# Kernel tuning notes

Measured on AMD Instinct MI355X. Metric: run time of the kernel, lower is better.

## Reference

```python
import jax, jax.numpy as jnp
import numpy as np

B, S, H, STEPS = 4096, 169, 64, 24  # batch, input seq (window 168 + covariate row), hidden, rollout steps


def _lstm(xseq, Wih, Whh, bih, bhh, h0, c0):
    """PyTorch-style single-layer LSTM. xseq: [B,T,D] -> ([B,T,H], hT, cT). Gate order i,f,g,o."""
    xg = jnp.einsum('btd,gd->btg', xseq, Wih) + (bih + bhh)  # precompute input proj [B,T,4H]

    def step(carry, xg_t):
        h, c = carry
        g = xg_t + h @ Whh.T
        i, f, gg, o = jnp.split(g, 4, axis=-1)
        c = jax.nn.sigmoid(f) * c + jax.nn.sigmoid(i) * jnp.tanh(gg)
        h = jax.nn.sigmoid(o) * jnp.tanh(c)
        return (h, c), h

    (hT, cT), hs = jax.lax.scan(step, (h0, c0), jnp.swapaxes(xg, 0, 1))
    return jnp.swapaxes(hs, 0, 1), hT, cT


def reference(x, Wih1, Whh1, bih1, bhh1, Wih2, Whh2, bih2, bhh2, fc1_w, fc1_b, fc2_w, fc2_b):
    win, d = x[:, :-1, :], x[:, -1, :]  # [B,168,1], [B,1]
    z = jnp.zeros((x.shape[0], H), x.dtype)

    def outer(win, _):
        h1s, h1, c1 = _lstm(win, Wih1, Whh1, bih1, bhh1, z, z)
        h1s = jax.nn.relu(h1s)
        # lstm2 is seeded with lstm1's final (h, c) state, as in the torch code
        h2s, _, _ = _lstm(h1s, Wih2, Whh2, bih2, bhh2, h1, c1)
        feat = jnp.concatenate([jax.nn.relu(h2s[:, -1, :]), d], axis=1)  # [B,65]
        out = (feat @ fc1_w.T + fc1_b) @ fc2_w.T + fc2_b  # [B,1] (no relu between fc1/fc2)
        win = jnp.concatenate([win[:, 1:, :], out[:, :, None]], axis=1)  # slide window
        return win, out[:, 0]

    _, outs = jax.lax.scan(outer, win, None, length=STEPS)  # outs: [24,B]
    return jnp.swapaxes(outs, 0, 1)  # [B,24]


def setup_inputs() -> dict:
    key = jax.random.key(0)
    ks = jax.random.split(key, 14)
    bnd = 1.0 / np.sqrt(H)

    def u(k, shape):
        return jax.random.uniform(k, shape, jnp.float32, -bnd, bnd)

    return {
        'x': jax.random.normal(ks[0], (B, S, 1), jnp.float32),
        'Wih1': u(ks[1], (4 * H, 1)),
        'Whh1': u(ks[2], (4 * H, H)),
        'bih1': u(ks[3], (4 * H,)),
        'bhh1': u(ks[4], (4 * H,)),
        'Wih2': u(ks[5], (4 * H, H)),
        'Whh2': u(ks[6], (4 * H, H)),
        'bih2': u(ks[7], (4 * H,)),
        'bhh2': u(ks[8], (4 * H,)),
        'fc1_w': u(ks[9], (64, 65)),
        'fc1_b': u(ks[10], (64,)),
        'fc2_w': u(ks[11], (1, 64)),
        'fc2_b': u(ks[12], (1,)),
    }
```

## Files before the change

### kernel.cpp

```cpp
#include <hip/hip_runtime.h>
#include <stdint.h>

#define NB 16
#define WIN 168
#define NSTEPS 24
#define NBLK (4096/NB)

typedef __attribute__((ext_vector_type(8))) short bf16x8;
typedef __attribute__((ext_vector_type(4))) float f32x4;

#if __has_builtin(__builtin_amdgcn_rcpf)
#define RCPF(x) __builtin_amdgcn_rcpf(x)
#else
#define RCPF(x) (1.0f / (x))
#endif
#if __has_builtin(__builtin_amdgcn_exp2f)
#define EXP2F(x) __builtin_amdgcn_exp2f(x)
#else
#define EXP2F(x) __expf((x) * 0.6931471805599453f)
#endif

__device__ __forceinline__ float sigm(float x){
  return RCPF(1.0f + EXP2F(x * -1.4426950408889634f));
}
__device__ __forceinline__ float tanh_(float x){
  return __builtin_fmaf(2.0f, RCPF(1.0f + EXP2F(x * -2.8853900817779268f)), -1.0f);
}

__device__ __forceinline__ uint32_t bf_rn(float f){
  uint32_t u = __builtin_bit_cast(uint32_t, f);
  return (u + 0x7FFFu + ((u >> 16) & 1u)) >> 16;
}
__device__ __forceinline__ float bf_f(uint32_t s){
  return __builtin_bit_cast(float, s << 16);
}
__device__ __forceinline__ void split_t(float f, uint32_t& hi, uint32_t& lo){
  uint32_t u = __builtin_bit_cast(uint32_t, f);
  hi = u >> 16;
  lo = bf_rn(f - bf_f(hi));
}
__device__ __forceinline__ void split_s(float f, short& hi, short& lo){
  uint32_t h = bf_rn(f);
  hi = (short)h;
  lo = (short)bf_rn(f - bf_f(h));
}
__device__ __forceinline__ f32x4 mfma16(bf16x8 a, bf16x8 b, f32x4 c){
  return __builtin_amdgcn_mfma_f32_16x16x32_bf16(a, b, c, 0, 0, 0);
}

__device__ __forceinline__ void lstm_epi(const f32x4 acc[4], float c[4], float hn[4]){
  #pragma unroll
  for (int r = 0; r < 4; r++){
    float gi = acc[0][r], gf = acc[1][r], gg = acc[2][r], go = acc[3][r];
    float cn = __builtin_fmaf(sigm(gf), c[r], sigm(gi) * tanh_(gg));
    c[r] = cn;
    hn[r] = sigm(go) * tanh_(cn);
  }
}

#define FROW 136
#define FBLK 544
#define FB(buf,hl,kt) ((((buf)*2 + (hl))*2 + (kt)) * FBLK)
#define BUF_INTS (2*FBLK)

template<bool FUSED>
__global__ __launch_bounds__(256, 1) void lstm_rec_kernel(
  const float* __restrict__ x,    const float* __restrict__ Wih1, const float* __restrict__ Whh1,
  const float* __restrict__ bih1, const float* __restrict__ bhh1,
  const float* __restrict__ Wih2, const float* __restrict__ Whh2,
  const float* __restrict__ bih2, const float* __restrict__ bhh2,
  const float* __restrict__ fc1w, const float* __restrict__ fc1b,
  const float* __restrict__ fc2w, const float* __restrict__ fc2b,
  float* __restrict__ out, short* __restrict__ hist)
{
  __shared__ __align__(16) short aS[2*2*2*FBLK];
  __shared__ __align__(16) short bS[FUSED ? 2*2*2*FBLK : 16];
  __shared__ __align__(16) short r1f[FUSED ? 16 : 2*2*2*FBLK];
  __shared__ __align__(16) short rlf[FUSED ? 16 : 2*2*2*FBLK];
  __shared__ float win_s[WIN][NB];
  __shared__ float Hlast[NB][68];
  __shared__ float fc1w_s[64*68];
  __shared__ float dval_s[NB];

  const int tid = threadIdx.x;
  const int wv  = tid >> 6;
  const int ln  = tid & 63;
  const int q   = ln >> 4;
  const int n   = ln & 15;
  const int bg0 = blockIdx.x * NB;
  const int u0  = 16*wv + 4*q;
  const int kt_  = u0 >> 5;
  const int q2_  = (u0 >> 3) & 3;
  const int jj0_ = u0 & 7;
  const int rdo  = q*FROW + n*8;
  const int wro  = q2_*FROW + n*8 + jj0_;
  const int gwo  = kt_*512 + q2_*128 + n*8 + jj0_;
  const int ro   = q*128 + n*8;
  short* __restrict__ hblk = FUSED ? (hist + (size_t)blockIdx.x * WIN * 2048) : nullptr;

  for (int i = tid; i < WIN*NB; i += 256){ int t = i >> 4, b = i & 15; win_s[t][b] = x[(bg0 + b)*169 + t]; }
  for (int i = tid; i < 64*65; i += 256){ int j = i / 65, k = i % 65; fc1w_s[j*68 + k] = fc1w[i]; }
  if (tid < NB) dval_s[tid] = x[(bg0 + tid)*169 + 168];

  const float fc1b_r = fc1b[ln];
  const float fc2w_r = fc2w[ln];
  const float fc2b_r = fc2b[0];

  bf16x8 A1hi[4][2], A1lo[4][2], Ain1[4];
  bf16x8 A2hi[4][4], A2lo[4][4];
  f32x4 b1c[4], b2c[4];
  #pragma unroll
  for (int e = 0; e < 4; e++){
    const int ja = 64*e + 16*wv + n;
    #pragma unroll
    for (int kt = 0; kt < 2; kt++){
      const float* p = Whh1 + ja*64 + kt*32 + q*8;
      #pragma unroll
      for (int jj = 0; jj < 8; jj++){ short h,l; split_s(p[jj], h, l); A1hi[e][kt][jj] = h; A1lo[e][kt][jj] = l; }
    }
    #pragma unroll
    for (int kt = 0; kt < 4; kt++){
      const float* p = (kt < 2 ? (Wih2 + ja*64 + kt*32) : (Whh2 + ja*64 + (kt-2)*32)) + q*8;
      #pragma unroll
      for (int jj = 0; jj < 8; jj++){ short h,l; split_s(p[jj], h, l); A2hi[e][kt][jj] = h; A2lo[e][kt][jj] = l; }
    }
    bf16x8 ain = {0,0,0,0,0,0,0,0};
    if (q == 0){ short wh, wl; split_s(Wih1[ja], wh, wl); ain[0] = wh; ain[1] = wh; ain[2] = wl; }
    Ain1[e] = ain;
    const int jc = 64*e + u0;
    #pragma unroll
    for (int r = 0; r < 4; r++){
      b1c[e][r] = bih1[jc+r] + bhh1[jc+r];
      b2c[e][r] = bih2[jc+r] + bhh2[jc+r];
    }
  }

  float c1[4], c2[4], c1r[4];

  auto lstm1_step = [&](short* S, float* cst, int rb, int wb, int slot, int relu_dst, int t, bool first){
    f32x4 acc[4];
    bf16x8 bin = {0,0,0,0,0,0,0,0};
    { float xv = win_s[slot][n]; uint32_t xh, xl; split_t(xv, xh, xl);
      if (q == 0){ bin[0] = (short)xh; bin[1] = (short)xl; bin[2] = (short)xh; } }
    if (first){
      #pragma unroll
      for (int e = 0; e < 4; e++) acc[e] = mfma16(Ain1[e], bin, b1c[e]);
    } else {
      bf16x8 Bh0 = *(const bf16x8*)&S[FB(rb,0,0)+rdo];
      bf16x8 Bl0 = *(const bf16x8*)&S[FB(rb,1,0)+rdo];
      bf16x8 Bh1 = *(const bf16x8*)&S[FB(rb,0,1)+rdo];
      bf16x8 Bl1 = *(const bf16x8*)&S[FB(rb,1,1)+rdo];
      #pragma unroll
      for (int e = 0; e < 4; e++){
        f32x4 a = b1c[e];
        a = mfma16(A1hi[e][0], Bh0, a);
        a = mfma16(A1hi[e][0], Bl0, a);
        a = mfma16(A1lo[e][0], Bh0, a);
        a = mfma16(A1hi[e][1], Bh1, a);
        a = mfma16(A1hi[e][1], Bl1, a);
        a = mfma16(A1lo[e][1], Bh1, a);
        a = mfma16(Ain1[e], bin, a);
        acc[e] = a;
      }
    }
    float hn[4];
    lstm_epi(acc, cst, hn);
    uint32_t ph[4], pl[4];
    #pragma unroll
    for (int r = 0; r < 4; r++) split_t(hn[r], ph[r], pl[r]);
    *(uint2*)&S[FB(wb,0,kt_)+wro] = make_uint2(ph[0] | (ph[1]<<16), ph[2] | (ph[3]<<16));
    *(uint2*)&S[FB(wb,1,kt_)+wro] = make_uint2(pl[0] | (pl[1]<<16), pl[2] | (pl[3]<<16));
    if (relu_dst){
      uint32_t sh[4], sl[4];
      #pragma unroll
      for (int r = 0; r < 4; r++){ bool pos = hn[r] > 0.0f; sh[r] = pos ? ph[r] : 0u; sl[r] = pos ? pl[r] : 0u; }
      uint2 phi = make_uint2(sh[0] | (sh[1]<<16), sh[2] | (sh[3]<<16));
      uint2 plo = make_uint2(sl[0] | (sl[1]<<16), sl[2] | (sl[3]<<16));
      if (relu_dst == 1){
        short* Hp = hblk + (size_t)t * 2048;
        *(uint2*)&Hp[gwo]        = phi;
        *(uint2*)&Hp[1024 + gwo] = plo;
      } else {
        *(uint2*)&rlf[FB(rb,0,kt_)+wro] = phi;
        *(uint2*)&rlf[FB(rb,1,kt_)+wro] = plo;
      }
    }
  };

  auto lstm2_core = [&](bf16x8 L1h0, bf16x8 L1l0, bf16x8 L1h1, bf16x8 L1l1,
                        const short* Sr, int rbuf, short* Sw, int wbuf, bool last){
    bf16x8 L2h0 = *(const bf16x8*)&Sr[FB(rbuf,0,0)+rdo];
    bf16x8 L2l0 = *(const bf16x8*)&Sr[FB(rbuf,1,0)+rdo];
    bf16x8 L2h1 = *(const bf16x8*)&Sr[FB(rbuf,0,1)+rdo];
    bf16x8 L2l1 = *(const bf16x8*)&Sr[FB(rbuf,1,1)+rdo];
    f32x4 acc[4];
    #pragma unroll
    for (int e = 0; e < 4; e++){
      f32x4 a = b2c[e];
      a = mfma16(A2hi[e][0], L1h0, a);
      a = mfma16(A2hi[e][0], L1l0, a);
      a = mfma16(A2lo[e][0], L1h0, a);
      a = mfma16(A2hi[e][1], L1h1, a);
      a = mfma16(A2hi[e][1], L1l1, a);
      a = mfma16(A2lo[e][1], L1h1, a);
      a = mfma16(A2hi[e][2], L2h0, a);
      a = mfma16(A2hi[e][2], L2l0, a);
      a = mfma16(A2lo[e][2], L2h0, a);
      a = mfma16(A2hi[e][3], L2h1, a);
      a = mfma16(A2hi[e][3], L2l1, a);
      a = mfma16(A2lo[e][3], L2h1, a);
      acc[e] = a;
    }
    float hn[4];
    lstm_epi(acc, c2, hn);
    if (!last){
      uint32_t ph[4], pl[4];
      #pragma unroll
      for (int r = 0; r < 4; r++) split_t(hn[r], ph[r], pl[r]);
      *(uint2*)&Sw[FB(wbuf,0,kt_)+wro] = make_uint2(ph[0] | (ph[1]<<16), ph[2] | (ph[3]<<16));
      *(uint2*)&Sw[FB(wbuf,1,kt_)+wro] = make_uint2(pl[0] | (pl[1]<<16), pl[2] | (pl[3]<<16));
    } else {
      #pragma unroll
      for (int r = 0; r < 4; r++) Hlast[n][u0 + r] = fmaxf(hn[r], 0.0f);
    }
  };

  auto hload = [&](int t, bf16x8& h0, bf16x8& l0, bf16x8& h1, bf16x8& l1){
    const short* Hp = hblk + (size_t)t * 2048;
    h0 = *(const bf16x8*)&Hp[ro];
    l0 = *(const bf16x8*)&Hp[1024 + ro];
    h1 = *(const bf16x8*)&Hp[512 + ro];
    l1 = *(const bf16x8*)&Hp[1536 + ro];
  };

  auto fc_head = [&](int s){
    float o4[4];
    #pragma unroll
    for (int bi = 0; bi < 4; bi++){
      const int b = 4*wv + bi;
      float a1 = fc1b_r;
      #pragma unroll
      for (int k4 = 0; k4 < 16; k4++){
        const float* wp = &fc1w_s[ln*68 + k4*4];
        const float* hp = &Hlast[b][k4*4];
        a1 += wp[0]*hp[0] + wp[1]*hp[1] + wp[2]*hp[2] + wp[3]*hp[3];
      }
      a1 += dval_s[b] * fc1w_s[ln*68 + 64];
      float v = a1 * fc2w_r;
      #pragma unroll
      for (int off = 32; off > 0; off >>= 1) v += __shfl_xor(v, off);
      o4[bi] = v + fc2b_r;
    }
    if (ln == 0){
      #pragma unroll
      for (int bi = 0; bi < 4; bi++){
        const int b = 4*wv + bi;
        out[(bg0 + b)*24 + s] = o4[bi];
        win_s[s % WIN][b] = o4[bi];
      }
    }
  };

  if constexpr (FUSED){
    #pragma unroll
    for (int r = 0; r < 4; r++) c1[r] = 0.0f;
    __syncthreads();
    lstm1_step(aS, c1, 0, 1, 0, 1, 0, true);
    for (int t = 1; t < WIN; t++){
      __syncthreads();
      lstm1_step(aS, c1, t & 1, (t & 1) ^ 1, t, 1, t, false);
    }

    for (int sg = 1; sg < NSTEPS; sg++){
      #pragma unroll
      for (int r = 0; r < 4; r++){ c2[r] = c1[r]; c1[r] = 0.0f; }
      bf16x8 ch0, cl0, ch1, cl1, nh0, nl0, nh1, nl1;
      hload(0, ch0, cl0, ch1, cl1);
      int slot = sg;
      hload(1, nh0, nl0, nh1, nl1);
      __syncthreads();
      lstm1_step(aS, c1, 0, 1, slot, 1, 0, true);
      lstm2_core(ch0, cl0, ch1, cl1, aS, 0, bS, 1, false);
      ch0 = nh0; cl0 = nl0; ch1 = nh1; cl1 = nl1;
      slot++; if (slot == WIN) slot = 0;
      for (int t = 1; t < WIN-1; t++){
        hload(t+1, nh0, nl0, nh1, nl1);
        __syncthreads();
        lstm1_step(aS, c1, t & 1, (t & 1) ^ 1, slot, 1, t, false);
        lstm2_core(ch0, cl0, ch1, cl1, bS, t & 1, bS, (t & 1) ^ 1, false);
        ch0 = nh0; cl0 = nl0; ch1 = nh1; cl1 = nl1;
        slot++; if (slot == WIN) slot = 0;
      }
      __syncthreads();
      lstm2_core(ch0, cl0, ch1, cl1, bS, 1, bS, 0, true);
      __syncthreads();
      fc_head(sg - 1);
      __syncthreads();
      lstm1_step(aS, c1, 1, 0, slot, 1, WIN-1, false);
    }

    #pragma unroll
    for (int r = 0; r < 4; r++) c2[r] = c1[r];
    {
      bf16x8 ch0, cl0, ch1, cl1, nh0, nl0, nh1, nl1;
      hload(0, ch0, cl0, ch1, cl1);
      hload(1, nh0, nl0, nh1, nl1);
      __syncthreads();
      lstm2_core(ch0, cl0, ch1, cl1, aS, 0, bS, 1, false);
      ch0 = nh0; cl0 = nl0; ch1 = nh1; cl1 = nl1;
      for (int t = 1; t < WIN; t++){
        if (t < WIN-1) hload(t+1, nh0, nl0, nh1, nl1);
        __syncthreads();
        lstm2_core(ch0, cl0, ch1, cl1, bS, t & 1, bS, (t & 1) ^ 1, t == WIN-1);
        ch0 = nh0; cl0 = nl0; ch1 = nh1; cl1 = nl1;
      }
      __syncthreads();
      fc_head(NSTEPS - 1);
    }
  } else {
    for (int s = 0; s < NSTEPS; s++){
      { int* p = (int*)&aS[0];
        for (int i = tid; i < BUF_INTS; i += 256) p[i] = 0; }
      #pragma unroll
      for (int r = 0; r < 4; r++) c1[r] = 0.0f;
      int slot = s;
      for (int t = 0; t < WIN; t++){
        __syncthreads();
        lstm1_step(aS, c1, t & 1, (t & 1) ^ 1, slot, 0, t, false);
        slot++; if (slot == WIN) slot = 0;
      }
      #pragma unroll
      for (int r = 0; r < 4; r++){ c2[r] = c1[r]; c1r[r] = 0.0f; }
      { int* p = (int*)&r1f[0];
        for (int i = tid; i < BUF_INTS; i += 256) p[i] = 0; }
      slot = s;
      __syncthreads();
      lstm1_step(r1f, c1r, 0, 1, slot, 2, 0, false);
      slot++;
      for (int i = 1; i < WIN; i++){
        __syncthreads();
        const int rb = i & 1, wb = rb ^ 1;
        lstm1_step(r1f, c1r, rb, wb, slot, 2, i, false);
        bf16x8 L1h0 = *(const bf16x8*)&rlf[FB(wb,0,0)+rdo];
        bf16x8 L1l0 = *(const bf16x8*)&rlf[FB(wb,1,0)+rdo];
        bf16x8 L1h1 = *(const bf16x8*)&rlf[FB(wb,0,1)+rdo];
        bf16x8 L1l1 = *(const bf16x8*)&rlf[FB(wb,1,1)+rdo];
        lstm2_core(L1h0, L1l0, L1h1, L1l1, aS, wb, aS, rb, false);
        slot++; if (slot == WIN) slot = 0;
      }
      __syncthreads();
      {
        const int rb = (WIN - 1) & 1;
        bf16x8 L1h0 = *(const bf16x8*)&rlf[FB(rb,0,0)+rdo];
        bf16x8 L1l0 = *(const bf16x8*)&rlf[FB(rb,1,0)+rdo];
        bf16x8 L1h1 = *(const bf16x8*)&rlf[FB(rb,0,1)+rdo];
        bf16x8 L1l1 = *(const bf16x8*)&rlf[FB(rb,1,1)+rdo];
        lstm2_core(L1h0, L1l0, L1h1, L1l1, aS, rb, aS, 0, true);
      }
      __syncthreads();
      fc_head(s);
    }
  }
}

extern "C" void kernel_launch(void* const* d_in, const int* in_sizes, int n_in,
                              void* d_out, int out_size, void* d_ws, size_t ws_size,
                              hipStream_t stream) {
  (void)in_sizes; (void)n_in; (void)out_size;
  const size_t need = (size_t)NBLK * WIN * 2048 * sizeof(short);
  if (ws_size >= need){
    lstm_rec_kernel<true><<<dim3(NBLK), dim3(256), 0, stream>>>(
        (const float*)d_in[0], (const float*)d_in[1], (const float*)d_in[2],
        (const float*)d_in[3], (const float*)d_in[4], (const float*)d_in[5],
        (const float*)d_in[6], (const float*)d_in[7], (const float*)d_in[8],
        (const float*)d_in[9], (const float*)d_in[10], (const float*)d_in[11],
        (const float*)d_in[12], (float*)d_out, (short*)d_ws);
  } else {
    lstm_rec_kernel<false><<<dim3(NBLK), dim3(256), 0, stream>>>(
        (const float*)d_in[0], (const float*)d_in[1], (const float*)d_in[2],
        (const float*)d_in[3], (const float*)d_in[4], (const float*)d_in[5],
        (const float*)d_in[6], (const float*)d_in[7], (const float*)d_in[8],
        (const float*)d_in[9], (const float*)d_in[10], (const float*)d_in[11],
        (const float*)d_in[12], (float*)d_out, (short*)nullptr);
  }
}
```

Before: 5.478 ms.

## Split LSTM1 and LSTM2 onto separate warp groups in a 512-thread block

The fused kernel now uses 512 threads per block. Waves 0-3 run layer 1 of the next rollout step while waves 4-7 run layer 2 of the current step, in lockstep through matched __syncthreads counts. The cell-state handoff goes through a shared cS array, and layer-1 outputs still travel through the global workspace. This is meant to halve the per-wave serial MFMA and epilogue chain per timestep and to cut register pressure, so the launch bound can ask for 2 blocks per CU. The cost is fragile barrier-count matching between the two warp groups, plus more LDS and more threads per block.

```diff
diff --git a/kernel.cpp b/kernel.cpp
--- a/kernel.cpp
+++ b/kernel.cpp
@@ -5,6 +5,7 @@
 #define WIN 168
 #define NSTEPS 24
 #define NBLK (4096/NB)
+#define NT 512
 
 typedef __attribute__((ext_vector_type(8))) short bf16x8;
 typedef __attribute__((ext_vector_type(4))) float f32x4;
@@ -63,8 +64,7 @@
 #define FB(buf,hl,kt) ((((buf)*2 + (hl))*2 + (kt)) * FBLK)
 #define BUF_INTS (2*FBLK)
 
-template<bool FUSED>
-__global__ __launch_bounds__(256, 1) void lstm_rec_kernel(
+__global__ __launch_bounds__(NT, 2) void lstm_fused_kernel(
   const float* __restrict__ x,    const float* __restrict__ Wih1, const float* __restrict__ Whh1,
   const float* __restrict__ bih1, const float* __restrict__ bhh1,
   const float* __restrict__ Wih2, const float* __restrict__ Whh2,
@@ -74,9 +74,289 @@
   float* __restrict__ out, short* __restrict__ hist)
 {
   __shared__ __align__(16) short aS[2*2*2*FBLK];
-  __shared__ __align__(16) short bS[FUSED ? 2*2*2*FBLK : 16];
-  __shared__ __align__(16) short r1f[FUSED ? 16 : 2*2*2*FBLK];
-  __shared__ __align__(16) short rlf[FUSED ? 16 : 2*2*2*FBLK];
+  __shared__ __align__(16) short bS[2*2*2*FBLK];
+  __shared__ float cS[64][16];
+  __shared__ float win_s[WIN][NB];
+  __shared__ float Hlast[NB][68];
+  __shared__ float fc1w_s[64*68];
+  __shared__ float dval_s[NB];
+
+  const int tid = threadIdx.x;
+  const int wv8 = tid >> 6;
+  const int wv  = wv8 & 3;
+  const bool isA = (wv8 < 4);
+  const int ln  = tid & 63;
+  const int q   = ln >> 4;
+  const int n   = ln & 15;
+  const int bg0 = blockIdx.x * NB;
+  const int u0  = 16*wv + 4*q;
+  const int kt_  = u0 >> 5;
+  const int q2_  = (u0 >> 3) & 3;
+  const int jj0_ = u0 & 7;
+  const int rdo  = q*FROW + n*8;
+  const int wro  = q2_*FROW + n*8 + jj0_;
+  const int gwo  = kt_*512 + q2_*128 + n*8 + jj0_;
+  const int ro   = q*128 + n*8;
+  short* __restrict__ hblk = hist + (size_t)blockIdx.x * WIN * 2048;
+
+  for (int i = tid; i < WIN*NB; i += NT){ int t = i >> 4, b = i & 15; win_s[t][b] = x[(bg0 + b)*169 + t]; }
+  for (int i = tid; i < 64*65; i += NT){ int j = i / 65, k = i % 65; fc1w_s[j*68 + k] = fc1w[i]; }
+  if (tid < NB) dval_s[tid] = x[(bg0 + tid)*169 + 168];
+
+  const float fc1b_r = fc1b[ln];
+  const float fc2w_r = fc2w[ln];
+  const float fc2b_r = fc2b[0];
+
+  auto fc_head = [&](int s){
+    float o2[2];
+    #pragma unroll
+    for (int bi = 0; bi < 2; bi++){
+      const int b = 2*wv8 + bi;
+      float a1 = fc1b_r;
+      #pragma unroll
+      for (int k4 = 0; k4 < 16; k4++){
+        const float* wp = &fc1w_s[ln*68 + k4*4];
+        const float* hp = &Hlast[b][k4*4];
+        a1 += wp[0]*hp[0] + wp[1]*hp[1] + wp[2]*hp[2] + wp[3]*hp[3];
+      }
+      a1 += dval_s[b] * fc1w_s[ln*68 + 64];
+      float v = a1 * fc2w_r;
+      #pragma unroll
+      for (int off = 32; off > 0; off >>= 1) v += __shfl_xor(v, off);
+      o2[bi] = v + fc2b_r;
+    }
+    if (ln == 0){
+      #pragma unroll
+      for (int bi = 0; bi < 2; bi++){
+        const int b = 2*wv8 + bi;
+        out[(bg0 + b)*24 + s] = o2[bi];
+        win_s[s % WIN][b] = o2[bi];
+      }
+    }
+  };
+
+  if (isA){
+    bf16x8 A1hi[4][2], A1lo[4][2], Ain1[4];
+    f32x4 b1c[4];
+    #pragma unroll
+    for (int e = 0; e < 4; e++){
+      const int ja = 64*e + 16*wv + n;
+      #pragma unroll
+      for (int kt = 0; kt < 2; kt++){
+        const float* p = Whh1 + ja*64 + kt*32 + q*8;
+        #pragma unroll
+        for (int jj = 0; jj < 8; jj++){ short h,l; split_s(p[jj], h, l); A1hi[e][kt][jj] = h; A1lo[e][kt][jj] = l; }
+      }
+      bf16x8 ain = {0,0,0,0,0,0,0,0};
+      if (q == 0){ short wh, wl; split_s(Wih1[ja], wh, wl); ain[0] = wh; ain[1] = wh; ain[2] = wl; }
+      Ain1[e] = ain;
+      const int jc = 64*e + u0;
+      #pragma unroll
+      for (int r = 0; r < 4; r++) b1c[e][r] = bih1[jc+r] + bhh1[jc+r];
+    }
+    float c1[4];
+
+    auto lstm1 = [&](int rb, int wb, int slot, int t, bool first){
+      f32x4 acc[4];
+      bf16x8 bin = {0,0,0,0,0,0,0,0};
+      { float xv = win_s[slot][n]; uint32_t xh, xl; split_t(xv, xh, xl);
+        if (q == 0){ bin[0] = (short)xh; bin[1] = (short)xl; bin[2] = (short)xh; } }
+      if (first){
+        #pragma unroll
+        for (int e = 0; e < 4; e++) acc[e] = mfma16(Ain1[e], bin, b1c[e]);
+      } else {
+        bf16x8 Bh0 = *(const bf16x8*)&aS[FB(rb,0,0)+rdo];
+        bf16x8 Bl0 = *(const bf16x8*)&aS[FB(rb,1,0)+rdo];
+        bf16x8 Bh1 = *(const bf16x8*)&aS[FB(rb,0,1)+rdo];
+        bf16x8 Bl1 = *(const bf16x8*)&aS[FB(rb,1,1)+rdo];
+        #pragma unroll
+        for (int e = 0; e < 4; e++){
+          f32x4 a = b1c[e];
+          a = mfma16(A1hi[e][0], Bh0, a);
+          a = mfma16(A1hi[e][0], Bl0, a);
+          a = mfma16(A1lo[e][0], Bh0, a);
+          a = mfma16(A1hi[e][1], Bh1, a);
+          a = mfma16(A1hi[e][1], Bl1, a);
+          a = mfma16(A1lo[e][1], Bh1, a);
+          a = mfma16(Ain1[e], bin, a);
+          acc[e] = a;
+        }
+      }
+      float hn[4];
+      lstm_epi(acc, c1, hn);
+      uint32_t ph[4], pl[4];
+      #pragma unroll
+      for (int r = 0; r < 4; r++) split_t(hn[r], ph[r], pl[r]);
+      *(uint2*)&aS[FB(wb,0,kt_)+wro] = make_uint2(ph[0] | (ph[1]<<16), ph[2] | (ph[3]<<16));
+      *(uint2*)&aS[FB(wb,1,kt_)+wro] = make_uint2(pl[0] | (pl[1]<<16), pl[2] | (pl[3]<<16));
+      uint32_t sh[4], sl[4];
+      #pragma unroll
+      for (int r = 0; r < 4; r++){ bool pos = hn[r] > 0.0f; sh[r] = pos ? ph[r] : 0u; sl[r] = pos ? pl[r] : 0u; }
+      short* Hp = hblk + (size_t)t * 2048;
+      *(uint2*)&Hp[gwo]        = make_uint2(sh[0] | (sh[1]<<16), sh[2] | (sh[3]<<16));
+      *(uint2*)&Hp[1024 + gwo] = make_uint2(sl[0] | (sl[1]<<16), sl[2] | (sl[3]<<16));
+    };
+
+    #pragma unroll
+    for (int r = 0; r < 4; r++) c1[r] = 0.0f;
+    for (int t = 0; t < WIN; t++){
+      __syncthreads();
+      lstm1(t & 1, (t & 1) ^ 1, t, t, t == 0);
+    }
+    #pragma unroll
+    for (int r = 0; r < 4; r++) cS[u0 + r][n] = c1[r];
+
+    for (int sg = 1; sg < NSTEPS; sg++){
+      #pragma unroll
+      for (int r = 0; r < 4; r++) c1[r] = 0.0f;
+      int slot = sg;
+      __syncthreads();
+      lstm1(0, 1, slot, 0, true);
+      slot++;
+      for (int t = 1; t < WIN-1; t++){
+        __syncthreads();
+        lstm1(t & 1, (t & 1) ^ 1, slot, t, false);
+        slot++; if (slot == WIN) slot = 0;
+      }
+      __syncthreads();
+      __syncthreads();
+      fc_head(sg - 1);
+      __syncthreads();
+      lstm1(1, 0, slot, WIN-1, false);
+      #pragma unroll
+      for (int r = 0; r < 4; r++) cS[u0 + r][n] = c1[r];
+    }
+
+    for (int i = 0; i < WIN + 1; i++) __syncthreads();
+    fc_head(NSTEPS - 1);
+
+  } else {
+    bf16x8 A2hi[4][4], A2lo[4][4];
+    f32x4 b2c[4];
+    #pragma unroll
+    for (int e = 0; e < 4; e++){
+      const int ja = 64*e + 16*wv + n;
+      #pragma unroll
+      for (int kt = 0; kt < 4; kt++){
+        const float* p = (kt < 2 ? (Wih2 + ja*64 + kt*32) : (Whh2 + ja*64 + (kt-2)*32)) + q*8;
+        #pragma unroll
+        for (int jj = 0; jj < 8; jj++){ short h,l; split_s(p[jj], h, l); A2hi[e][kt][jj] = h; A2lo[e][kt][jj] = l; }
+      }
+      const int jc = 64*e + u0;
+      #pragma unroll
+      for (int r = 0; r < 4; r++) b2c[e][r] = bih2[jc+r] + bhh2[jc+r];
+    }
+    float c2[4];
+    bf16x8 ch0, cl0, ch1, cl1, nh0, nl0, nh1, nl1;
+
+    auto loadc = [&](int t){
+      const short* Hp = hblk + (size_t)t * 2048;
+      ch0 = *(const bf16x8*)&Hp[ro];
+      cl0 = *(const bf16x8*)&Hp[1024 + ro];
+      ch1 = *(const bf16x8*)&Hp[512 + ro];
+      cl1 = *(const bf16x8*)&Hp[1536 + ro];
+    };
+    auto loadn = [&](int t){
+      const short* Hp = hblk + (size_t)t * 2048;
+      nh0 = *(const bf16x8*)&Hp[ro];
+      nl0 = *(const bf16x8*)&Hp[1024 + ro];
+      nh1 = *(const bf16x8*)&Hp[512 + ro];
+      nl1 = *(const bf16x8*)&Hp[1536 + ro];
+    };
+    auto shift = [&](){ ch0 = nh0; cl0 = nl0; ch1 = nh1; cl1 = nl1; };
+
+    auto lstm2 = [&](const short* Sr, int rb, short* Sw, int wb, bool last){
+      bf16x8 L2h0 = *(const bf16x8*)&Sr[FB(rb,0,0)+rdo];
+      bf16x8 L2l0 = *(const bf16x8*)&Sr[FB(rb,1,0)+rdo];
+      bf16x8 L2h1 = *(const bf16x8*)&Sr[FB(rb,0,1)+rdo];
+      bf16x8 L2l1 = *(const bf16x8*)&Sr[FB(rb,1,1)+rdo];
+      f32x4 acc[4];
+      #pragma unroll
+      for (int e = 0; e < 4; e++){
+        f32x4 a = b2c[e];
+        a = mfma16(A2hi[e][0], ch0, a);
+        a = mfma16(A2hi[e][0], cl0, a);
+        a = mfma16(A2lo[e][0], ch0, a);
+        a = mfma16(A2hi[e][1], ch1, a);
+        a = mfma16(A2hi[e][1], cl1, a);
+        a = mfma16(A2lo[e][1], ch1, a);
+        a = mfma16(A2hi[e][2], L2h0, a);
+        a = mfma16(A2hi[e][2], L2l0, a);
+        a = mfma16(A2lo[e][2], L2h0, a);
+        a = mfma16(A2hi[e][3], L2h1, a);
+        a = mfma16(A2hi[e][3], L2l1, a);
+        a = mfma16(A2lo[e][3], L2h1, a);
+        acc[e] = a;
+      }
+      float hn[4];
+      lstm_epi(acc, c2, hn);
+      if (!last){
+        uint32_t ph[4], pl[4];
+        #pragma unroll
+        for (int r = 0; r < 4; r++) split_t(hn[r], ph[r], pl[r]);
+        *(uint2*)&Sw[FB(wb,0,kt_)+wro] = make_uint2(ph[0] | (ph[1]<<16), ph[2] | (ph[3]<<16));
+        *(uint2*)&Sw[FB(wb,1,kt_)+wro] = make_uint2(pl[0] | (pl[1]<<16), pl[2] | (pl[3]<<16));
+      } else {
+        #pragma unroll
+        for (int r = 0; r < 4; r++) Hlast[n][u0 + r] = fmaxf(hn[r], 0.0f);
+      }
+    };
+
+    for (int i = 0; i < WIN; i++) __syncthreads();
+
+    for (int sg = 1; sg < NSTEPS; sg++){
+      loadc(0);
+      loadn(1);
+      __syncthreads();
+      #pragma unroll
+      for (int r = 0; r < 4; r++) c2[r] = cS[u0 + r][n];
+      lstm2(aS, 0, bS, 1, false);
+      shift();
+      for (int t = 1; t < WIN-1; t++){
+        loadn(t + 1);
+        __syncthreads();
+        lstm2(bS, t & 1, bS, (t & 1) ^ 1, false);
+        shift();
+      }
+      __syncthreads();
+      lstm2(bS, 1, bS, 0, true);
+      __syncthreads();
+      fc_head(sg - 1);
+      __syncthreads();
+    }
+
+    {
+      loadc(0);
+      loadn(1);
+      __syncthreads();
+      #pragma unroll
+      for (int r = 0; r < 4; r++) c2[r] = cS[u0 + r][n];
+      lstm2(aS, 0, bS, 1, false);
+      shift();
+      for (int t = 1; t < WIN; t++){
+        if (t < WIN-1) loadn(t + 1);
+        __syncthreads();
+        lstm2(bS, t & 1, bS, (t & 1) ^ 1, t == WIN-1);
+        shift();
+      }
+      __syncthreads();
+      fc_head(NSTEPS - 1);
+    }
+  }
+}
+
+__global__ __launch_bounds__(256, 1) void lstm_fallback_kernel(
+  const float* __restrict__ x,    const float* __restrict__ Wih1, const float* __restrict__ Whh1,
+  const float* __restrict__ bih1, const float* __restrict__ bhh1,
+  const float* __restrict__ Wih2, const float* __restrict__ Whh2,
+  const float* __restrict__ bih2, const float* __restrict__ bhh2,
+  const float* __restrict__ fc1w, const float* __restrict__ fc1b,
+  const float* __restrict__ fc2w, const float* __restrict__ fc2b,
+  float* __restrict__ out)
+{
+  __shared__ __align__(16) short aS[2*2*2*FBLK];
+  __shared__ __align__(16) short r1f[2*2*2*FBLK];
+  __shared__ __align__(16) short rlf[2*2*2*FBLK];
   __shared__ float win_s[WIN][NB];
   __shared__ float Hlast[NB][68];
   __shared__ float fc1w_s[64*68];
@@ -94,9 +374,6 @@
   const int jj0_ = u0 & 7;
   const int rdo  = q*FROW + n*8;
   const int wro  = q2_*FROW + n*8 + jj0_;
-  const int gwo  = kt_*512 + q2_*128 + n*8 + jj0_;
-  const int ro   = q*128 + n*8;
-  short* __restrict__ hblk = FUSED ? (hist + (size_t)blockIdx.x * WIN * 2048) : nullptr;
 
   for (int i = tid; i < WIN*NB; i += 256){ int t = i >> 4, b = i & 15; win_s[t][b] = x[(bg0 + b)*169 + t]; }
   for (int i = tid; i < 64*65; i += 256){ int j = i / 65, k = i % 65; fc1w_s[j*68 + k] = fc1w[i]; }
@@ -137,31 +414,26 @@
 
   float c1[4], c2[4], c1r[4];
 
-  auto lstm1_step = [&](short* S, float* cst, int rb, int wb, int slot, int relu_dst, int t, bool first){
-    f32x4 acc[4];
+  auto lstm1_step = [&](short* S, float* cst, int rb, int wb, int slot, bool relu_out){
+    bf16x8 Bh0 = *(const bf16x8*)&S[FB(rb,0,0)+rdo];
+    bf16x8 Bl0 = *(const bf16x8*)&S[FB(rb,1,0)+rdo];
+    bf16x8 Bh1 = *(const bf16x8*)&S[FB(rb,0,1)+rdo];
+    bf16x8 Bl1 = *(const bf16x8*)&S[FB(rb,1,1)+rdo];
     bf16x8 bin = {0,0,0,0,0,0,0,0};
     { float xv = win_s[slot][n]; uint32_t xh, xl; split_t(xv, xh, xl);
       if (q == 0){ bin[0] = (short)xh; bin[1] = (short)xl; bin[2] = (short)xh; } }
-    if (first){
-      #pragma unroll
-      for (int e = 0; e < 4; e++) acc[e] = mfma16(Ain1[e], bin, b1c[e]);
-    } else {
-      bf16x8 Bh0 = *(const bf16x8*)&S[FB(rb,0,0)+rdo];
-      bf16x8 Bl0 = *(const bf16x8*)&S[FB(rb,1,0)+rdo];
-      bf16x8 Bh1 = *(const bf16x8*)&S[FB(rb,0,1)+rdo];
-      bf16x8 Bl1 = *(const bf16x8*)&S[FB(rb,1,1)+rdo];
-      #pragma unroll
-      for (int e = 0; e < 4; e++){
-        f32x4 a = b1c[e];
-        a = mfma16(A1hi[e][0], Bh0, a);
-        a = mfma16(A1hi[e][0], Bl0, a);
-        a = mfma16(A1lo[e][0], Bh0, a);
-        a = mfma16(A1hi[e][1], Bh1, a);
-        a = mfma16(A1hi[e][1], Bl1, a);
-        a = mfma16(A1lo[e][1], Bh1, a);
-        a = mfma16(Ain1[e], bin, a);
-        acc[e] = a;
-      }
+    f32x4 acc[4];
+    #pragma unroll
+    for (int e = 0; e < 4; e++){
+      f32x4 a = b1c[e];
+      a = mfma16(A1hi[e][0], Bh0, a);
+      a = mfma16(A1hi[e][0], Bl0, a);
+      a = mfma16(A1lo[e][0], Bh0, a);
+      a = mfma16(A1hi[e][1], Bh1, a);
+      a = mfma16(A1hi[e][1], Bl1, a);
+      a = mfma16(A1lo[e][1], Bh1, a);
+      a = mfma16(Ain1[e], bin, a);
+      acc[e] = a;
     }
     float hn[4];
     lstm_epi(acc, cst, hn);
@@ -170,29 +442,21 @@
     for (int r = 0; r < 4; r++) split_t(hn[r], ph[r], pl[r]);
     *(uint2*)&S[FB(wb,0,kt_)+wro] = make_uint2(ph[0] | (ph[1]<<16), ph[2] | (ph[3]<<16));
     *(uint2*)&S[FB(wb,1,kt_)+wro] = make_uint2(pl[0] | (pl[1]<<16), pl[2] | (pl[3]<<16));
-    if (relu_dst){
+    if (relu_out){
       uint32_t sh[4], sl[4];
       #pragma unroll
       for (int r = 0; r < 4; r++){ bool pos = hn[r] > 0.0f; sh[r] = pos ? ph[r] : 0u; sl[r] = pos ? pl[r] : 0u; }
-      uint2 phi = make_uint2(sh[0] | (sh[1]<<16), sh[2] | (sh[3]<<16));
-      uint2 plo = make_uint2(sl[0] | (sl[1]<<16), sl[2] | (sl[3]<<16));
-      if (relu_dst == 1){
-        short* Hp = hblk + (size_t)t * 2048;
-        *(uint2*)&Hp[gwo]        = phi;
-        *(uint2*)&Hp[1024 + gwo] = plo;
-      } else {
-        *(uint2*)&rlf[FB(rb,0,kt_)+wro] = phi;
-        *(uint2*)&rlf[FB(rb,1,kt_)+wro] = plo;
-      }
+      *(uint2*)&rlf[FB(rb,0,kt_)+wro] = make_uint2(sh[0] | (sh[1]<<16), sh[2] | (sh[3]<<16));
+      *(uint2*)&rlf[FB(rb,1,kt_)+wro] = make_uint2(sl[0] | (sl[1]<<16), sl[2] | (sl[3]<<16));
     }
   };
 
   auto lstm2_core = [&](bf16x8 L1h0, bf16x8 L1l0, bf16x8 L1h1, bf16x8 L1l1,
-                        const short* Sr, int rbuf, short* Sw, int wbuf, bool last){
-    bf16x8 L2h0 = *(const bf16x8*)&Sr[FB(rbuf,0,0)+rdo];
-    bf16x8 L2l0 = *(const bf16x8*)&Sr[FB(rbuf,1,0)+rdo];
-    bf16x8 L2h1 = *(const bf16x8*)&Sr[FB(rbuf,0,1)+rdo];
-    bf16x8 L2l1 = *(const bf16x8*)&Sr[FB(rbuf,1,1)+rdo];
+                        int rbuf, int wbuf, bool last){
+    bf16x8 L2h0 = *(const bf16x8*)&aS[FB(rbuf,0,0)+rdo];
+    bf16x8 L2l0 = *(const bf16x8*)&aS[FB(rbuf,1,0)+rdo];
+    bf16x8 L2h1 = *(const bf16x8*)&aS[FB(rbuf,0,1)+rdo];
+    bf16x8 L2l1 = *(const bf16x8*)&aS[FB(rbuf,1,1)+rdo];
     f32x4 acc[4];
     #pragma unroll
     for (int e = 0; e < 4; e++){
@@ -217,148 +481,80 @@
       uint32_t ph[4], pl[4];
       #pragma unroll
       for (int r = 0; r < 4; r++) split_t(hn[r], ph[r], pl[r]);
-      *(uint2*)&Sw[FB(wbuf,0,kt_)+wro] = make_uint2(ph[0] | (ph[1]<<16), ph[2] | (ph[3]<<16));
-      *(uint2*)&Sw[FB(wbuf,1,kt_)+wro] = make_uint2(pl[0] | (pl[1]<<16), pl[2] | (pl[3]<<16));
+      *(uint2*)&aS[FB(wbuf,0,kt_)+wro] = make_uint2(ph[0] | (ph[1]<<16), ph[2] | (ph[3]<<16));
+      *(uint2*)&aS[FB(wbuf,1,kt_)+wro] = make_uint2(pl[0] | (pl[1]<<16), pl[2] | (pl[3]<<16));
     } else {
       #pragma unroll
       for (int r = 0; r < 4; r++) Hlast[n][u0 + r] = fmaxf(hn[r], 0.0f);
     }
   };
 
-  auto hload = [&](int t, bf16x8& h0, bf16x8& l0, bf16x8& h1, bf16x8& l1){
-    const short* Hp = hblk + (size_t)t * 2048;
-    h0 = *(const bf16x8*)&Hp[ro];
-    l0 = *(const bf16x8*)&Hp[1024 + ro];
-    h1 = *(const bf16x8*)&Hp[512 + ro];
-    l1 = *(const bf16x8*)&Hp[1536 + ro];
-  };
-
-  auto fc_head = [&](int s){
-    float o4[4];
-    #pragma unroll
-    for (int bi = 0; bi < 4; bi++){
-      const int b = 4*wv + bi;
-      float a1 = fc1b_r;
-      #pragma unroll
-      for (int k4 = 0; k4 < 16; k4++){
-        const float* wp = &fc1w_s[ln*68 + k4*4];
-        const float* hp = &Hlast[b][k4*4];
-        a1 += wp[0]*hp[0] + wp[1]*hp[1] + wp[2]*hp[2] + wp[3]*hp[3];
-      }
-      a1 += dval_s[b] * fc1w_s[ln*68 + 64];
-      float v = a1 * fc2w_r;
-      #pragma unroll
-      for (int off = 32; off > 0; off >>= 1) v += __shfl_xor(v, off);
-      o4[bi] = v + fc2b_r;
-    }
-    if (ln == 0){
+  for (int s = 0; s < NSTEPS; s++){
+    { int* p = (int*)&aS[0];
+      for (int i = tid; i < BUF_INTS; i += 256) p[i] = 0; }
+    #pragma unroll
+    for (int r = 0; r < 4; r++) c1[r] = 0.0f;
+    int slot = s;
+    for (int t = 0; t < WIN; t++){
+      __syncthreads();
+      lstm1_step(aS, c1, t & 1, (t & 1) ^ 1, slot, false);
+      slot++; if (slot == WIN) slot = 0;
+    }
+    #pragma unroll
+    for (int r = 0; r < 4; r++){ c2[r] = c1[r]; c1r[r] = 0.0f; }
+    { int* p = (int*)&r1f[0];
+      for (int i = tid; i < BUF_INTS; i += 256) p[i] = 0; }
+    slot = s;
+    __syncthreads();
+    lstm1_step(r1f, c1r, 0, 1, slot, true);
+    slot++;
+    for (int i = 1; i < WIN; i++){
+      __syncthreads();
+      const int rb = i & 1, wb = rb ^ 1;
+      lstm1_step(r1f, c1r, rb, wb, slot, true);
+      bf16x8 L1h0 = *(const bf16x8*)&rlf[FB(wb,0,0)+rdo];
+      bf16x8 L1l0 = *(const bf16x8*)&rlf[FB(wb,1,0)+rdo];
+      bf16x8 L1h1 = *(const bf16x8*)&rlf[FB(wb,0,1)+rdo];
+      bf16x8 L1l1 = *(const bf16x8*)&rlf[FB(wb,1,1)+rdo];
+      lstm2_core(L1h0, L1l0, L1h1, L1l1, wb, rb, false);
+      slot++; if (slot == WIN) slot = 0;
+    }
+    __syncthreads();
+    {
+      const int rb = (WIN - 1) & 1;
+      bf16x8 L1h0 = *(const bf16x8*)&rlf[FB(rb,0,0)+rdo];
+      bf16x8 L1l0 = *(const bf16x8*)&rlf[FB(rb,1,0)+rdo];
+      bf16x8 L1h1 = *(const bf16x8*)&rlf[FB(rb,0,1)+rdo];
+      bf16x8 L1l1 = *(const bf16x8*)&rlf[FB(rb,1,1)+rdo];
+      lstm2_core(L1h0, L1l0, L1h1, L1l1, rb, 0, true);
+    }
+    __syncthreads();
+    {
+      float o4[4];
       #pragma unroll
       for (int bi = 0; bi < 4; bi++){
         const int b = 4*wv + bi;
-        out[(bg0 + b)*24 + s] = o4[bi];
-        win_s[s % WIN][b] = o4[bi];
-      }
-    }
-  };
-
-  if constexpr (FUSED){
-    #pragma unroll
-    for (int r = 0; r < 4; r++) c1[r] = 0.0f;
-    __syncthreads();
-    lstm1_step(aS, c1, 0, 1, 0, 1, 0, true);
-    for (int t = 1; t < WIN; t++){
-      __syncthreads();
-      lstm1_step(aS, c1, t & 1, (t & 1) ^ 1, t, 1, t, false);
-    }
-
-    for (int sg = 1; sg < NSTEPS; sg++){
-      #pragma unroll
-      for (int r = 0; r < 4; r++){ c2[r] = c1[r]; c1[r] = 0.0f; }
-      bf16x8 ch0, cl0, ch1, cl1, nh0, nl0, nh1, nl1;
-      hload(0, ch0, cl0, ch1, cl1);
-      int slot = sg;
-      hload(1, nh0, nl0, nh1, nl1);
-      __syncthreads();
-      lstm1_step(aS, c1, 0, 1, slot, 1, 0, true);
-      lstm2_core(ch0, cl0, ch1, cl1, aS, 0, bS, 1, false);
-      ch0 = nh0; cl0 = nl0; ch1 = nh1; cl1 = nl1;
-      slot++; if (slot == WIN) slot = 0;
-      for (int t = 1; t < WIN-1; t++){
-        hload(t+1, nh0, nl0, nh1, nl1);
-        __syncthreads();
-        lstm1_step(aS, c1, t & 1, (t & 1) ^ 1, slot, 1, t, false);
-        lstm2_core(ch0, cl0, ch1, cl1, bS, t & 1, bS, (t & 1) ^ 1, false);
-        ch0 = nh0; cl0 = nl0; ch1 = nh1; cl1 = nl1;
-        slot++; if (slot == WIN) slot = 0;
-      }
-      __syncthreads();
-      lstm2_core(ch0, cl0, ch1, cl1, bS, 1, bS, 0, true);
-      __syncthreads();
-      fc_head(sg - 1);
-      __syncthreads();
-      lstm1_step(aS, c1, 1, 0, slot, 1, WIN-1, false);
-    }
-
-    #pragma unroll
-    for (int r = 0; r < 4; r++) c2[r] = c1[r];
-    {
-      bf16x8 ch0, cl0, ch1, cl1, nh0, nl0, nh1, nl1;
-      hload(0, ch0, cl0, ch1, cl1);
-      hload(1, nh0, nl0, nh1, nl1);
-      __syncthreads();
-      lstm2_core(ch0, cl0, ch1, cl1, aS, 0, bS, 1, false);
-      ch0 = nh0; cl0 = nl0; ch1 = nh1; cl1 = nl1;
-      for (int t = 1; t < WIN; t++){
-        if (t < WIN-1) hload(t+1, nh0, nl0, nh1, nl1);
-        __syncthreads();
-        lstm2_core(ch0, cl0, ch1, cl1, bS, t & 1, bS, (t & 1) ^ 1, t == WIN-1);
-        ch0 = nh0; cl0 = nl0; ch1 = nh1; cl1 = nl1;
-      }
-      __syncthreads();
-      fc_head(NSTEPS - 1);
-    }
-  } else {
-    for (int s = 0; s < NSTEPS; s++){
-      { int* p = (int*)&aS[0];
-        for (int i = tid; i < BUF_INTS; i += 256) p[i] = 0; }
-      #pragma unroll
-      for (int r = 0; r < 4; r++) c1[r] = 0.0f;
-      int slot = s;
-      for (int t = 0; t < WIN; t++){
-        __syncthreads();
-        lstm1_step(aS, c1, t & 1, (t & 1) ^ 1, slot, 0, t, false);
-        slot++; if (slot == WIN) slot = 0;
-      }
-      #pragma unroll
-      for (int r = 0; r < 4; r++){ c2[r] = c1[r]; c1r[r] = 0.0f; }
-      { int* p = (int*)&r1f[0];
-        for (int i = tid; i < BUF_INTS; i += 256) p[i] = 0; }
-      slot = s;
-      __syncthreads();
-      lstm1_step(r1f, c1r, 0, 1, slot, 2, 0, false);
-      slot++;
-      for (int i = 1; i < WIN; i++){
-        __syncthreads();
-        const int rb = i & 1, wb = rb ^ 1;
-        lstm1_step(r1f, c1r, rb, wb, slot, 2, i, false);
-        bf16x8 L1h0 = *(const bf16x8*)&rlf[FB(wb,0,0)+rdo];
-        bf16x8 L1l0 = *(const bf16x8*)&rlf[FB(wb,1,0)+rdo];
-        bf16x8 L1h1 = *(const bf16x8*)&rlf[FB(wb,0,1)+rdo];
-        bf16x8 L1l1 = *(const bf16x8*)&rlf[FB(wb,1,1)+rdo];
-        lstm2_core(L1h0, L1l0, L1h1, L1l1, aS, wb, aS, rb, false);
-        slot++; if (slot == WIN) slot = 0;
-      }
-      __syncthreads();
-      {
-        const int rb = (WIN - 1) & 1;
-        bf16x8 L1h0 = *(const bf16x8*)&rlf[FB(rb,0,0)+rdo];
-        bf16x8 L1l0 = *(const bf16x8*)&rlf[FB(rb,1,0)+rdo];
-        bf16x8 L1h1 = *(const bf16x8*)&rlf[FB(rb,0,1)+rdo];
-        bf16x8 L1l1 = *(const bf16x8*)&rlf[FB(rb,1,1)+rdo];
-        lstm2_core(L1h0, L1l0, L1h1, L1l1, aS, rb, aS, 0, true);
-      }
-      __syncthreads();
-      fc_head(s);
+        float a1 = fc1b_r;
+        #pragma unroll
+        for (int k4 = 0; k4 < 16; k4++){
+          const float* wp = &fc1w_s[ln*68 + k4*4];
+          const float* hp = &Hlast[b][k4*4];
+          a1 += wp[0]*hp[0] + wp[1]*hp[1] + wp[2]*hp[2] + wp[3]*hp[3];
+        }
+        a1 += dval_s[b] * fc1w_s[ln*68 + 64];
+        float v = a1 * fc2w_r;
+        #pragma unroll
+        for (int off = 32; off > 0; off >>= 1) v += __shfl_xor(v, off);
+        o4[bi] = v + fc2b_r;
+      }
+      if (ln == 0){
+        #pragma unroll
+        for (int bi = 0; bi < 4; bi++){
+          const int b = 4*wv + bi;
+          out[(bg0 + b)*24 + s] = o4[bi];
+          win_s[s % WIN][b] = o4[bi];
+        }
+      }
     }
   }
 }
@@ -369,18 +565,18 @@
   (void)in_sizes; (void)n_in; (void)out_size;
   const size_t need = (size_t)NBLK * WIN * 2048 * sizeof(short);
   if (ws_size >= need){
-    lstm_rec_kernel<true><<<dim3(NBLK), dim3(256), 0, stream>>>(
+    lstm_fused_kernel<<<dim3(NBLK), dim3(NT), 0, stream>>>(
         (const float*)d_in[0], (const float*)d_in[1], (const float*)d_in[2],
         (const float*)d_in[3], (const float*)d_in[4], (const float*)d_in[5],
         (const float*)d_in[6], (const float*)d_in[7], (const float*)d_in[8],
         (const float*)d_in[9], (const float*)d_in[10], (const float*)d_in[11],
         (const float*)d_in[12], (float*)d_out, (short*)d_ws);
   } else {
-    lstm_rec_kernel<false><<<dim3(NBLK), dim3(256), 0, stream>>>(
+    lstm_fallback_kernel<<<dim3(NBLK), dim3(256), 0, stream>>>(
         (const float*)d_in[0], (const float*)d_in[1], (const float*)d_in[2],
         (const float*)d_in[3], (const float*)d_in[4], (const float*)d_in[5],
         (const float*)d_in[6], (const float*)d_in[7], (const float*)d_in[8],
         (const float*)d_in[9], (const float*)d_in[10], (const float*)d_in[11],
-        (const float*)d_in[12], (float*)d_out, (short*)nullptr);
+        (const float*)d_in[12], (float*)d_out);
   }
 }
```

Measured after the change: 5.020 ms. 8.4% less time.
